# Performance work log

Measured on AMD Instinct MI355X. Metric: run time of the kernel, lower is better.

The kernel has to match this reference:

```python
import jax, jax.numpy as jnp
import numpy as np
from jax import lax

_MS_SSIM_WEIGHTS = [0.0448, 0.2856, 0.3001, 0.2363, 0.1333]
LEVELS = 5
WINDOW_SIZE = 11
SIGMA = 1.5
DATA_RANGE = 2.0


def _gaussian_kernel(size, sigma, channels):
    x = jnp.arange(size, dtype=jnp.float32) - size // 2
    g = jnp.exp(-x ** 2 / (2.0 * sigma ** 2))
    g = g / g.sum()
    k2d = jnp.outer(g, g)  # [size, size]
    # depthwise kernel: [C, 1, size, size] (OIHW with feature_group_count=C)
    return jnp.broadcast_to(k2d[None, None], (channels, 1, size, size))


def _depthwise_conv(x, kernel, pad):
    C = x.shape[1]
    return lax.conv_general_dilated(
        x, kernel,
        window_strides=(1, 1),
        padding=[(pad, pad), (pad, pad)],
        dimension_numbers=('NCHW', 'OIHW', 'NCHW'),
        feature_group_count=C)


def _avg_pool2(x):
    s = lax.reduce_window(x, 0.0, lax.add, (1, 1, 2, 2), (1, 1, 2, 2), 'VALID')
    return s * 0.25


def _ssim(x, y, window_size=WINDOW_SIZE, sigma=SIGMA, data_range=DATA_RANGE):
    K1, K2 = 0.01, 0.03
    C1 = (K1 * data_range) ** 2
    C2 = (K2 * data_range) ** 2
    kernel = _gaussian_kernel(window_size, sigma, x.shape[1])
    pad = window_size // 2
    mu1 = _depthwise_conv(x, kernel, pad)
    mu2 = _depthwise_conv(y, kernel, pad)
    mu1_sq = mu1 * mu1
    mu2_sq = mu2 * mu2
    mu1_mu2 = mu1 * mu2
    sig1_sq = _depthwise_conv(x * x, kernel, pad) - mu1_sq
    sig2_sq = _depthwise_conv(y * y, kernel, pad) - mu2_sq
    sig12 = _depthwise_conv(x * y, kernel, pad) - mu1_mu2
    num = (2.0 * mu1_mu2 + C1) * (2.0 * sig12 + C2)
    den = (mu1_sq + mu2_sq + C1) * (sig1_sq + sig2_sq + C2)
    ssim_map = num / (den + 1e-8)
    return ssim_map.mean()


def setup_inputs() -> dict:
    key = jax.random.key(0)
    k1, k2 = jax.random.split(key)
    pred = jax.random.normal(k1, (16, 3, 512, 512), dtype=jnp.float32)
    target = jax.random.normal(k2, (16, 3, 512, 512), dtype=jnp.float32)
    return {"pred": pred, "target": target}


def reference(pred, target):
    weights = jnp.asarray(_MS_SSIM_WEIGHTS[:LEVELS], dtype=jnp.float32)
    weights = weights / weights.sum()
    ms_ssim_val = jnp.zeros((), dtype=jnp.float32)
    x, y = pred, target
    for i in range(LEVELS):
        s = _ssim(x, y)
        ms_ssim_val = ms_ssim_val + weights[i] * s
        if i < LEVELS - 1:
            x = _avg_pool2(x)
            y = _avg_pool2(y)
    return 1.0 - ms_ssim_val
```

## Files before the change

### kernel.cpp

```cpp
#include <hip/hip_runtime.h>


#define TW 64
#define NIMG 48
#define P2 63
#define P1 62
#define NSLOT 256
#define SSTRIDE 16

typedef float v2f __attribute__((ext_vector_type(2)));

template <int TH>
__global__ __launch_bounds__(256, 2) void ssim_level_kernel(
    const float* __restrict__ x, const float* __restrict__ y,
    long imgStride, int rowStride,
    float* __restrict__ dsx, float* __restrict__ dsy,
    long dsImgStride, int dsRowStride,
    const float* __restrict__ zpad,
    float* __restrict__ slots, int H, int W, int pad, int do_ds)
{
    constexpr int HHALO = TH + 10;
    constexpr int RPT   = TH / 4;

    const float G[11] = {
        0.00102839f, 0.00759877f, 0.03600077f, 0.10936069f, 0.21300539f,
        0.26601173f, 0.21300539f, 0.10936069f, 0.03600077f, 0.00759877f,
        0.00102839f};
    const float C1 = 4.0e-4f;
    const float C2 = 3.6e-3f;

    __shared__ __align__(16) v2f   sm01[HHALO * P2];
    __shared__ __align__(16) v2f   sm23[HHALO * P2];
    __shared__ __align__(16) float sm4 [HHALO * P1];

    const int t   = threadIdx.x;
    const int img = blockIdx.z;
    const int C0  = blockIdx.x * TW;
    const int R0  = blockIdx.y * TH;
    const float* xi = x + (long)img * imgStride;
    const float* yi = y + (long)img * imgStride;

    if (do_ds) {
        const int dsW = W >> 1, dsH = H >> 1;
        const long dbase = (long)img * dsImgStride;
        for (int i = t; i < (TH / 2) * 32; i += 256) {
            const int dr = i >> 5, dc = i & 31;
            const int gr2 = (R0 >> 1) + dr;
            const int gc2 = (C0 >> 1) + dc;
            if (gr2 < dsH && gc2 < dsW) {
                const float* sx = xi + (long)(2 * gr2) * rowStride + 2 * gc2;
                const float* sy = yi + (long)(2 * gr2) * rowStride + 2 * gc2;
                const float2 a0 = *reinterpret_cast<const float2*>(sx);
                const float2 a1 = *reinterpret_cast<const float2*>(sx + rowStride);
                const float2 b0 = *reinterpret_cast<const float2*>(sy);
                const float2 b1 = *reinterpret_cast<const float2*>(sy + rowStride);
                const long o = dbase + (long)gr2 * dsRowStride + gc2;
                dsx[o] = 0.25f * (a0.x + a0.y + a1.x + a1.y);
                dsy[o] = 0.25f * (b0.x + b0.y + b1.x + b1.y);
            }
            if (gr2 < dsH && dc < 8) {
                if (blockIdx.x == 0) {
                    const long o = dbase + (long)gr2 * dsRowStride + (dc - 8);
                    dsx[o] = 0.0f; dsy[o] = 0.0f;
                }
                if (blockIdx.x == gridDim.x - 1) {
                    const long o = dbase + (long)gr2 * dsRowStride + (dsW + dc);
                    dsx[o] = 0.0f; dsy[o] = 0.0f;
                }
            }
        }
    }

    const bool fastp = pad || ((C0 >= 8) && (C0 + TW + 8 <= W));
    for (int s = t; s < HHALO * 8; s += 256) {
        const int r  = s % HHALO;
        const int q  = s / HHALO;
        const int gr = R0 + r - 5;
        const bool rok = ((unsigned)gr < (unsigned)H);
        const int gc0 = C0 + (q << 3) - 8;

        float xv[24], yv[24];
        if (fastp) {
            const float* px = rok ? (xi + (long)gr * rowStride + gc0) : zpad;
            const float* py = rok ? (yi + (long)gr * rowStride + gc0) : zpad;
#pragma unroll
            for (int v = 0; v < 6; ++v) {
                const float4 a = reinterpret_cast<const float4*>(px)[v];
                const float4 b = reinterpret_cast<const float4*>(py)[v];
                xv[4 * v + 0] = a.x; xv[4 * v + 1] = a.y;
                xv[4 * v + 2] = a.z; xv[4 * v + 3] = a.w;
                yv[4 * v + 0] = b.x; yv[4 * v + 1] = b.y;
                yv[4 * v + 2] = b.z; yv[4 * v + 3] = b.w;
            }
        } else {
            const float* xrow = xi + (long)gr * rowStride;
            const float* yrow = yi + (long)gr * rowStride;
#pragma unroll
            for (int k = 3; k < 21; ++k) {
                const int gc = gc0 + k;
                const bool ok = rok && ((unsigned)gc < (unsigned)W);
                xv[k] = ok ? xrow[gc] : 0.0f;
                yv[k] = ok ? yrow[gc] : 0.0f;
            }
        }

        v2f w2[18]; float xy[18];
#pragma unroll
        for (int k = 0; k < 18; ++k) {
            const float a = xv[k + 3], b = yv[k + 3];
            v2f w; w.x = a * a; w.y = b * b;
            w2[k] = w; xy[k] = a * b;
        }

        const int cb = (q << 3);
#pragma unroll
        for (int j = 0; j < 8; ++j) {
            v2f s01 = {0.f, 0.f}, s23 = {0.f, 0.f};
            float s4 = 0.f;
#pragma unroll
            for (int k = 0; k < 11; ++k) {
                const float g = G[k];
                v2f w; w.x = xv[j + k + 3]; w.y = yv[j + k + 3];
                s01 += w * g;
                s23 += w2[j + k] * g;
                s4   = fmaf(g, xy[j + k], s4);
            }
            sm01[r * P2 + cb + j] = s01;
            sm23[r * P2 + cb + j] = s23;
            sm4 [r * P1 + cb + j] = s4;
        }
    }
    __syncthreads();

    const int c   = t & 63;
    const int rr0 = (t >> 6) * RPT;
    v2f acc01[RPT], acc23[RPT];
    float acc4[RPT];
    {
        v2f hv[RPT + 10];
#pragma unroll
        for (int k = 0; k < RPT + 10; ++k) hv[k] = sm01[(rr0 + k) * P2 + c];
#pragma unroll
        for (int i = 0; i < RPT; ++i) {
            v2f a = {0.f, 0.f};
#pragma unroll
            for (int k = 0; k < 11; ++k) a += hv[i + k] * G[k];
            acc01[i] = a;
        }
#pragma unroll
        for (int k = 0; k < RPT + 10; ++k) hv[k] = sm23[(rr0 + k) * P2 + c];
#pragma unroll
        for (int i = 0; i < RPT; ++i) {
            v2f a = {0.f, 0.f};
#pragma unroll
            for (int k = 0; k < 11; ++k) a += hv[i + k] * G[k];
            acc23[i] = a;
        }
    }
    {
        float hs[RPT + 10];
#pragma unroll
        for (int k = 0; k < RPT + 10; ++k) hs[k] = sm4[(rr0 + k) * P1 + c];
#pragma unroll
        for (int i = 0; i < RPT; ++i) {
            float a = 0.f;
#pragma unroll
            for (int k = 0; k < 11; ++k) a = fmaf(G[k], hs[i + k], a);
            acc4[i] = a;
        }
    }

    float local = 0.f;
    const int gc = C0 + c;
#pragma unroll
    for (int i = 0; i < RPT; ++i) {
        const int gr2 = R0 + rr0 + i;
        if (gr2 < H && gc < W) {
            const float mu1 = acc01[i].x, mu2 = acc01[i].y;
            const float mu1s = mu1 * mu1, mu2s = mu2 * mu2, m12 = mu1 * mu2;
            const float s1  = acc23[i].x - mu1s;
            const float s2  = acc23[i].y - mu2s;
            const float s12 = acc4[i] - m12;
            const float num = (2.f * m12 + C1) * (2.f * s12 + C2);
            const float den = (mu1s + mu2s + C1) * (s1 + s2 + C2);
            local += num * __builtin_amdgcn_rcpf(den + 1e-8f);
        }
    }

#pragma unroll
    for (int off = 32; off > 0; off >>= 1) local += __shfl_down(local, off, 64);
    if ((t & 63) == 0) {
        const int bid = (blockIdx.z * gridDim.y + blockIdx.y) * gridDim.x + blockIdx.x;
        const int slot = ((bid << 2) | (t >> 6)) & (NSLOT - 1);
        atomicAdd(slots + slot * SSTRIDE, local);
    }
}

__global__ void finalize_kernel(const float* __restrict__ slots,
                                float* __restrict__ out)
{
    const int t = threadIdx.x;
    const float w[5] = {0.0448f, 0.2856f, 0.3001f, 0.2363f, 0.1333f};
    const float wsum = w[0] + w[1] + w[2] + w[3] + w[4];
    float acc = 0.f;
#pragma unroll
    for (int lvl = 0; lvl < 5; ++lvl) {
        const int d = 512 >> lvl;
        const float cnt = (float)NIMG * (float)d * (float)d;
        acc += (w[lvl] / wsum) / cnt * slots[(lvl * NSLOT + t) * SSTRIDE];
    }
#pragma unroll
    for (int off = 32; off > 0; off >>= 1) acc += __shfl_down(acc, off, 64);
    __shared__ float p[4];
    if ((t & 63) == 0) p[t >> 6] = acc;
    __syncthreads();
    if (t == 0) out[0] = 1.0f - (p[0] + p[1] + p[2] + p[3]);
}

extern "C" void kernel_launch(void* const* d_in, const int* in_sizes, int n_in,
                              void* d_out, int out_size, void* d_ws, size_t ws_size,
                              hipStream_t stream)
{
    const float* pred = (const float*)d_in[0];
    const float* targ = (const float*)d_in[1];
    float* out = (float*)d_out;
    float* ws  = (float*)d_ws;

    const long S1 = 256L * 272, S2 = 128L * 144, S3 = 64L * 80, S4 = 32L * 48;

    float* slots = ws;
    float* zpad  = slots + 5 * NSLOT * SSTRIDE;
    float* x1 = zpad + 640;
    float* y1 = x1 + NIMG * S1;
    float* x2 = y1 + NIMG * S1;
    float* y2 = x2 + NIMG * S2;
    float* x3 = y2 + NIMG * S2;
    float* y3 = x3 + NIMG * S3;
    float* x4 = y3 + NIMG * S3;
    float* y4 = x4 + NIMG * S4;

    hipMemsetAsync(ws, 0, (size_t)(5 * NSLOT * SSTRIDE + 640) * sizeof(float), stream);

    { dim3 g(8, 16, NIMG);
      ssim_level_kernel<32><<<g, 256, 0, stream>>>(pred, targ, 512L * 512, 512,
          x1 + 8, y1 + 8, S1, 272, zpad, slots + 0 * NSLOT * SSTRIDE, 512, 512, 0, 1); }
    { dim3 g(4, 8, NIMG);
      ssim_level_kernel<32><<<g, 256, 0, stream>>>(x1 + 8, y1 + 8, S1, 272,
          x2 + 8, y2 + 8, S2, 144, zpad, slots + 1 * NSLOT * SSTRIDE, 256, 256, 1, 1); }
    { dim3 g(2, 16, NIMG);
      ssim_level_kernel<8><<<g, 256, 0, stream>>>(x2 + 8, y2 + 8, S2, 144,
          x3 + 8, y3 + 8, S3, 80, zpad, slots + 2 * NSLOT * SSTRIDE, 128, 128, 1, 1); }
    { dim3 g(1, 8, NIMG);
      ssim_level_kernel<8><<<g, 256, 0, stream>>>(x3 + 8, y3 + 8, S3, 80,
          x4 + 8, y4 + 8, S4, 48, zpad, slots + 3 * NSLOT * SSTRIDE, 64, 64, 1, 1); }
    { dim3 g(1, 4, NIMG);
      ssim_level_kernel<8><<<g, 256, 0, stream>>>(x4 + 8, y4 + 8, S4, 48,
          nullptr, nullptr, 0, 0, zpad, slots + 4 * NSLOT * SSTRIDE, 32, 32, 1, 0); }

    finalize_kernel<<<1, 256, 0, stream>>>(slots, out);
}
```

Measured before the change: 283.6 us.

## Fuse pyramid pooling into level-0 kernel and merge remaining levels into one launch

The level-0 SSIM kernel now streams 128-row strips with a 42-row ring buffer in shared memory and fuses the four-level 2x2 average-pool pyramid into a single pass using shuffles. Levels 1-4 are merged into one launch with a flattened tile index. The three horizontal-conv planes are packed into a single float4 (x, y, x²+y², xy) with XOR swizzling, and the block size drops to 128 threads. The intent is to cut launch count, repeated downsample reads and halo recomputation, at the cost of more barriers per strip and lower per-block parallelism.

```diff
diff --git a/kernel.cpp b/kernel.cpp
--- a/kernel.cpp
+++ b/kernel.cpp
@@ -1,198 +1,342 @@
 #include <hip/hip_runtime.h>
 
 
-#define TW 64
+#define TW 32
+#define NTHR 128
 #define NIMG 48
-#define P2 63
-#define P1 62
+#define WIN 42
+#define PQ  32
 #define NSLOT 256
 #define SSTRIDE 16
 
-typedef float v2f __attribute__((ext_vector_type(2)));
-
-template <int TH>
-__global__ __launch_bounds__(256, 2) void ssim_level_kernel(
+#define RS1 272
+#define RS2 144
+#define RS3 80
+#define RS4 48
+#define IS0 (512L*512)
+#define IS1 (256L*272)
+#define IS2 (128L*144)
+#define IS3 (64L*80)
+#define IS4 (32L*48)
+
+typedef float v4f __attribute__((ext_vector_type(4)));
+
+struct Pyr {
+    float *x1, *y1, *x2, *y2, *x3, *y3, *x4, *y4;
+};
+
+__device__ __forceinline__ void h_load(
+    const float* __restrict__ xi, const float* __restrict__ yi,
+    const float* __restrict__ zpad, int gr, int gc0, int H, int W,
+    bool fastp, int rowStride, float* xv, float* yv)
+{
+    const bool rok = ((unsigned)gr < (unsigned)H);
+    if (fastp) {
+        const float* px = rok ? (xi + (long)gr * rowStride + gc0) : zpad;
+        const float* py = rok ? (yi + (long)gr * rowStride + gc0) : zpad;
+#pragma unroll
+        for (int v = 0; v < 6; ++v) {
+            const float4 a = reinterpret_cast<const float4*>(px)[v];
+            const float4 b = reinterpret_cast<const float4*>(py)[v];
+            xv[4*v+0]=a.x; xv[4*v+1]=a.y; xv[4*v+2]=a.z; xv[4*v+3]=a.w;
+            yv[4*v+0]=b.x; yv[4*v+1]=b.y; yv[4*v+2]=b.z; yv[4*v+3]=b.w;
+        }
+    } else {
+        const float* xrow = xi + (long)gr * rowStride;
+        const float* yrow = yi + (long)gr * rowStride;
+#pragma unroll
+        for (int k = 3; k < 21; ++k) {
+            const int gc = gc0 + k;
+            const bool ok = rok && ((unsigned)gc < (unsigned)W);
+            xv[k] = ok ? xrow[gc] : 0.0f;
+            yv[k] = ok ? yrow[gc] : 0.0f;
+        }
+    }
+}
+
+__device__ __forceinline__ void h_conv_write(
+    const float* xv, const float* yv, v4f* smA, int slot, int cb,
+    const float* G)
+{
+    v4f s[8];
+#pragma unroll
+    for (int j = 0; j < 8; ++j) s[j] = {0.f, 0.f, 0.f, 0.f};
+#pragma unroll
+    for (int m = 0; m < 18; ++m) {
+        const float a = xv[m+3], b = yv[m+3];
+        v4f w; w.x = a; w.y = b; w.z = a*a + b*b; w.w = a*b;
+#pragma unroll
+        for (int j = 0; j < 8; ++j) {
+            if (j <= m && m - j <= 10) {
+                s[j] += w * G[m - j];
+            }
+        }
+    }
+    const int u = slot & 31;
+#pragma unroll
+    for (int j = 0; j < 8; ++j)
+        smA[slot * PQ + ((cb + j) ^ u)] = s[j];
+}
+
+__device__ __forceinline__ float v_phase(
+    const v4f* smA, int vb, int c, int rr0, int R0, int C0, int H, int W,
+    const float* G)
+{
+    const float C1 = 4.0e-4f;
+    const float C2 = 3.6e-3f;
+    v4f acc[8];
+#pragma unroll
+    for (int i = 0; i < 8; ++i) acc[i] = {0.f, 0.f, 0.f, 0.f};
+    int sl = vb;
+#pragma unroll
+    for (int k = 0; k < 18; ++k) {
+        const v4f h = smA[sl * PQ + (c ^ (sl & 31))];
+#pragma unroll
+        for (int i = 0; i < 8; ++i) {
+            if (i <= k && k - i <= 10) {
+                acc[i] += h * G[k - i];
+            }
+        }
+        sl = (sl + 1 == WIN) ? 0 : sl + 1;
+    }
+    float local = 0.f;
+    const int gc = C0 + c;
+#pragma unroll
+    for (int i = 0; i < 8; ++i) {
+        const int gr2 = R0 + rr0 + i;
+        if (gr2 < H && gc < W) {
+            const float mu1 = acc[i].x, mu2 = acc[i].y;
+            const float mu1s = mu1*mu1, mu2s = mu2*mu2, m12 = mu1*mu2;
+            const float ssum = acc[i].z - mu1s - mu2s;
+            const float s12  = acc[i].w - m12;
+            const float num = (2.f * m12 + C1) * (2.f * s12 + C2);
+            const float den = (mu1s + mu2s + C1) * (ssum + C2);
+            local += num * __builtin_amdgcn_rcpf(den + 1e-8f);
+        }
+    }
+    return local;
+}
+
+__device__ __forceinline__ void pool_tree(
+    const float* __restrict__ xi, const float* __restrict__ yi,
+    int t, int R0, int C0, int z, const Pyr& p, int bx)
+{
+    const int r = t >> 3, c2 = t & 7;
+    const int gr = R0 + 4 * r;
+    const int gc = C0 + 4 * c2;
+
+    float4 ax[4], ay[4];
+#pragma unroll
+    for (int rr = 0; rr < 4; ++rr) {
+        ax[rr] = *reinterpret_cast<const float4*>(xi + (long)(gr+rr)*512 + gc);
+        ay[rr] = *reinterpret_cast<const float4*>(yi + (long)(gr+rr)*512 + gc);
+    }
+    float qx[2][2], qy[2][2];
+#pragma unroll
+    for (int i = 0; i < 2; ++i) {
+        qx[i][0] = 0.25f*(ax[2*i].x+ax[2*i].y+ax[2*i+1].x+ax[2*i+1].y);
+        qx[i][1] = 0.25f*(ax[2*i].z+ax[2*i].w+ax[2*i+1].z+ax[2*i+1].w);
+        qy[i][0] = 0.25f*(ay[2*i].x+ay[2*i].y+ay[2*i+1].x+ay[2*i+1].y);
+        qy[i][1] = 0.25f*(ay[2*i].z+ay[2*i].w+ay[2*i+1].z+ay[2*i+1].w);
+    }
+    float* x1p = p.x1 + z*IS1;  float* y1p = p.y1 + z*IS1;
+    float* x2p = p.x2 + z*IS2;  float* y2p = p.y2 + z*IS2;
+    float* x3p = p.x3 + z*IS3;  float* y3p = p.y3 + z*IS3;
+    float* x4p = p.x4 + z*IS4;  float* y4p = p.y4 + z*IS4;
+
+    const int r1 = (R0 >> 1) + 2*r, c1 = (C0 >> 1) + 2*c2;
+#pragma unroll
+    for (int i = 0; i < 2; ++i) {
+        *reinterpret_cast<float2*>(x1p + (long)(r1+i)*RS1 + c1) =
+            make_float2(qx[i][0], qx[i][1]);
+        *reinterpret_cast<float2*>(y1p + (long)(r1+i)*RS1 + c1) =
+            make_float2(qy[i][0], qy[i][1]);
+    }
+    const float v2x = 0.25f*(qx[0][0]+qx[0][1]+qx[1][0]+qx[1][1]);
+    const float v2y = 0.25f*(qy[0][0]+qy[0][1]+qy[1][0]+qy[1][1]);
+    x2p[(long)((R0>>2)+r)*RS2 + (C0>>2)+c2] = v2x;
+    y2p[(long)((R0>>2)+r)*RS2 + (C0>>2)+c2] = v2y;
+    const float v3x = 0.25f*(v2x + __shfl_down(v2x,1,64)
+                           + __shfl_down(v2x,8,64) + __shfl_down(v2x,9,64));
+    const float v3y = 0.25f*(v2y + __shfl_down(v2y,1,64)
+                           + __shfl_down(v2y,8,64) + __shfl_down(v2y,9,64));
+    if (!(r & 1) && !(c2 & 1)) {
+        x3p[(long)((R0>>3)+(r>>1))*RS3 + (C0>>3)+(c2>>1)] = v3x;
+        y3p[(long)((R0>>3)+(r>>1))*RS3 + (C0>>3)+(c2>>1)] = v3y;
+    }
+    const float v4x = 0.25f*(v3x + __shfl_down(v3x,2,64)
+                           + __shfl_down(v3x,16,64) + __shfl_down(v3x,18,64));
+    const float v4y = 0.25f*(v3y + __shfl_down(v3y,2,64)
+                           + __shfl_down(v3y,16,64) + __shfl_down(v3y,18,64));
+    if (!(r & 3) && !(c2 & 3)) {
+        x4p[(long)((R0>>4)+(r>>2))*RS4 + (C0>>4)+(c2>>2)] = v4x;
+        y4p[(long)((R0>>4)+(r>>2))*RS4 + (C0>>4)+(c2>>2)] = v4y;
+    }
+    if (bx == 0) {
+#pragma unroll
+        for (int i = 0; i < 2; ++i) {
+            x1p[(long)(r1+i)*RS1 + (c2-8)] = 0.f;
+            y1p[(long)(r1+i)*RS1 + (c2-8)] = 0.f;
+        }
+        x2p[(long)((R0>>2)+r)*RS2 + (c2-8)] = 0.f;
+        y2p[(long)((R0>>2)+r)*RS2 + (c2-8)] = 0.f;
+        if (r < 4) { x3p[(long)((R0>>3)+r)*RS3 + (c2-8)] = 0.f;
+                     y3p[(long)((R0>>3)+r)*RS3 + (c2-8)] = 0.f; }
+        if (r < 2) { x4p[(long)((R0>>4)+r)*RS4 + (c2-8)] = 0.f;
+                     y4p[(long)((R0>>4)+r)*RS4 + (c2-8)] = 0.f; }
+    }
+    if (bx == 15) {
+#pragma unroll
+        for (int i = 0; i < 2; ++i) {
+            x1p[(long)(r1+i)*RS1 + 256 + c2] = 0.f;
+            y1p[(long)(r1+i)*RS1 + 256 + c2] = 0.f;
+        }
+        x2p[(long)((R0>>2)+r)*RS2 + 128 + c2] = 0.f;
+        y2p[(long)((R0>>2)+r)*RS2 + 128 + c2] = 0.f;
+        if (r < 4) { x3p[(long)((R0>>3)+r)*RS3 + 64 + c2] = 0.f;
+                     y3p[(long)((R0>>3)+r)*RS3 + 64 + c2] = 0.f; }
+        if (r < 2) { x4p[(long)((R0>>4)+r)*RS4 + 32 + c2] = 0.f;
+                     y4p[(long)((R0>>4)+r)*RS4 + 32 + c2] = 0.f; }
+    }
+}
+
+__global__ __launch_bounds__(NTHR, 2) void ssim_l0_kernel(
     const float* __restrict__ x, const float* __restrict__ y,
-    long imgStride, int rowStride,
-    float* __restrict__ dsx, float* __restrict__ dsy,
-    long dsImgStride, int dsRowStride,
-    const float* __restrict__ zpad,
-    float* __restrict__ slots, int H, int W, int pad, int do_ds)
-{
-    constexpr int HHALO = TH + 10;
-    constexpr int RPT   = TH / 4;
-
+    Pyr p, const float* __restrict__ zpad, float* __restrict__ slots)
+{
     const float G[11] = {
         0.00102839f, 0.00759877f, 0.03600077f, 0.10936069f, 0.21300539f,
         0.26601173f, 0.21300539f, 0.10936069f, 0.03600077f, 0.00759877f,
         0.00102839f};
-    const float C1 = 4.0e-4f;
-    const float C2 = 3.6e-3f;
-
-    __shared__ __align__(16) v2f   sm01[HHALO * P2];
-    __shared__ __align__(16) v2f   sm23[HHALO * P2];
-    __shared__ __align__(16) float sm4 [HHALO * P1];
-
-    const int t   = threadIdx.x;
-    const int img = blockIdx.z;
-    const int C0  = blockIdx.x * TW;
-    const int R0  = blockIdx.y * TH;
-    const float* xi = x + (long)img * imgStride;
-    const float* yi = y + (long)img * imgStride;
-
-    if (do_ds) {
-        const int dsW = W >> 1, dsH = H >> 1;
-        const long dbase = (long)img * dsImgStride;
-        for (int i = t; i < (TH / 2) * 32; i += 256) {
-            const int dr = i >> 5, dc = i & 31;
-            const int gr2 = (R0 >> 1) + dr;
-            const int gc2 = (C0 >> 1) + dc;
-            if (gr2 < dsH && gc2 < dsW) {
-                const float* sx = xi + (long)(2 * gr2) * rowStride + 2 * gc2;
-                const float* sy = yi + (long)(2 * gr2) * rowStride + 2 * gc2;
-                const float2 a0 = *reinterpret_cast<const float2*>(sx);
-                const float2 a1 = *reinterpret_cast<const float2*>(sx + rowStride);
-                const float2 b0 = *reinterpret_cast<const float2*>(sy);
-                const float2 b1 = *reinterpret_cast<const float2*>(sy + rowStride);
-                const long o = dbase + (long)gr2 * dsRowStride + gc2;
-                dsx[o] = 0.25f * (a0.x + a0.y + a1.x + a1.y);
-                dsy[o] = 0.25f * (b0.x + b0.y + b1.x + b1.y);
-            }
-            if (gr2 < dsH && dc < 8) {
-                if (blockIdx.x == 0) {
-                    const long o = dbase + (long)gr2 * dsRowStride + (dc - 8);
-                    dsx[o] = 0.0f; dsy[o] = 0.0f;
-                }
-                if (blockIdx.x == gridDim.x - 1) {
-                    const long o = dbase + (long)gr2 * dsRowStride + (dsW + dc);
-                    dsx[o] = 0.0f; dsy[o] = 0.0f;
-                }
-            }
-        }
-    }
-
-    const bool fastp = pad || ((C0 >= 8) && (C0 + TW + 8 <= W));
-    for (int s = t; s < HHALO * 8; s += 256) {
-        const int r  = s % HHALO;
-        const int q  = s / HHALO;
-        const int gr = R0 + r - 5;
-        const bool rok = ((unsigned)gr < (unsigned)H);
-        const int gc0 = C0 + (q << 3) - 8;
-
+
+    __shared__ __align__(16) v4f smA[WIN * PQ];
+
+    const int t    = threadIdx.x;
+    const int bid  = blockIdx.x;
+    const int tile = (bid & 7) * 384 + (bid >> 3);
+    const int bx   = tile & 15;
+    const int by   = (tile >> 4) & 3;
+    const int z    = tile >> 6;
+    const int C0   = bx * TW;
+    const int S0   = by * 128;
+    const float* xi = x + (long)z * IS0;
+    const float* yi = y + (long)z * IS0;
+    const bool fastp = (C0 >= 8) && (C0 + TW + 8 <= 512);
+
+    for (int s = t; s < WIN * 4; s += NTHR) {
+        const int r = s % WIN, q = s / WIN;
+        float pxv[24], pyv[24];
+        h_load(xi, yi, zpad, S0 + r - 5, C0 + (q << 3) - 8, 512, 512, fastp,
+               512, pxv, pyv);
+        h_conv_write(pxv, pyv, smA, r, q << 3, G);
+    }
+    __syncthreads();
+
+    const int c    = t & 31;
+    const int rr0  = (t >> 5) * 8;
+    const int hr   = t & 31, hq = t >> 5;
+    const int hgc0 = C0 + (hq << 3) - 8;
+    int wslot = hr, vb = rr0;
+    float local = 0.f;
+
+    for (int tt = 0; tt < 3; ++tt) {
+        const int R0 = S0 + 32 * tt;
         float xv[24], yv[24];
-        if (fastp) {
-            const float* px = rok ? (xi + (long)gr * rowStride + gc0) : zpad;
-            const float* py = rok ? (yi + (long)gr * rowStride + gc0) : zpad;
-#pragma unroll
-            for (int v = 0; v < 6; ++v) {
-                const float4 a = reinterpret_cast<const float4*>(px)[v];
-                const float4 b = reinterpret_cast<const float4*>(py)[v];
-                xv[4 * v + 0] = a.x; xv[4 * v + 1] = a.y;
-                xv[4 * v + 2] = a.z; xv[4 * v + 3] = a.w;
-                yv[4 * v + 0] = b.x; yv[4 * v + 1] = b.y;
-                yv[4 * v + 2] = b.z; yv[4 * v + 3] = b.w;
-            }
-        } else {
-            const float* xrow = xi + (long)gr * rowStride;
-            const float* yrow = yi + (long)gr * rowStride;
-#pragma unroll
-            for (int k = 3; k < 21; ++k) {
-                const int gc = gc0 + k;
-                const bool ok = rok && ((unsigned)gc < (unsigned)W);
-                xv[k] = ok ? xrow[gc] : 0.0f;
-                yv[k] = ok ? yrow[gc] : 0.0f;
-            }
-        }
-
-        v2f w2[18]; float xy[18];
-#pragma unroll
-        for (int k = 0; k < 18; ++k) {
-            const float a = xv[k + 3], b = yv[k + 3];
-            v2f w; w.x = a * a; w.y = b * b;
-            w2[k] = w; xy[k] = a * b;
-        }
-
-        const int cb = (q << 3);
-#pragma unroll
-        for (int j = 0; j < 8; ++j) {
-            v2f s01 = {0.f, 0.f}, s23 = {0.f, 0.f};
-            float s4 = 0.f;
-#pragma unroll
-            for (int k = 0; k < 11; ++k) {
-                const float g = G[k];
-                v2f w; w.x = xv[j + k + 3]; w.y = yv[j + k + 3];
-                s01 += w * g;
-                s23 += w2[j + k] * g;
-                s4   = fmaf(g, xy[j + k], s4);
-            }
-            sm01[r * P2 + cb + j] = s01;
-            sm23[r * P2 + cb + j] = s23;
-            sm4 [r * P1 + cb + j] = s4;
-        }
-    }
-    __syncthreads();
-
-    const int c   = t & 63;
-    const int rr0 = (t >> 6) * RPT;
-    v2f acc01[RPT], acc23[RPT];
-    float acc4[RPT];
+        h_load(xi, yi, zpad, R0 + 37 + hr, hgc0, 512, 512, fastp, 512, xv, yv);
+        local += v_phase(smA, vb, c, rr0, R0, C0, 512, 512, G);
+        if (t < 64) pool_tree(xi, yi, t, R0, C0, z, p, bx);
+        __syncthreads();
+        h_conv_write(xv, yv, smA, wslot, hq << 3, G);
+        __syncthreads();
+        wslot += 32; if (wslot >= WIN) wslot -= WIN;
+        vb    += 32; if (vb    >= WIN) vb    -= WIN;
+    }
     {
-        v2f hv[RPT + 10];
-#pragma unroll
-        for (int k = 0; k < RPT + 10; ++k) hv[k] = sm01[(rr0 + k) * P2 + c];
-#pragma unroll
-        for (int i = 0; i < RPT; ++i) {
-            v2f a = {0.f, 0.f};
-#pragma unroll
-            for (int k = 0; k < 11; ++k) a += hv[i + k] * G[k];
-            acc01[i] = a;
-        }
-#pragma unroll
-        for (int k = 0; k < RPT + 10; ++k) hv[k] = sm23[(rr0 + k) * P2 + c];
-#pragma unroll
-        for (int i = 0; i < RPT; ++i) {
-            v2f a = {0.f, 0.f};
-#pragma unroll
-            for (int k = 0; k < 11; ++k) a += hv[i + k] * G[k];
-            acc23[i] = a;
-        }
-    }
-    {
-        float hs[RPT + 10];
-#pragma unroll
-        for (int k = 0; k < RPT + 10; ++k) hs[k] = sm4[(rr0 + k) * P1 + c];
-#pragma unroll
-        for (int i = 0; i < RPT; ++i) {
-            float a = 0.f;
-#pragma unroll
-            for (int k = 0; k < 11; ++k) a = fmaf(G[k], hs[i + k], a);
-            acc4[i] = a;
-        }
-    }
-
-    float local = 0.f;
-    const int gc = C0 + c;
-#pragma unroll
-    for (int i = 0; i < RPT; ++i) {
-        const int gr2 = R0 + rr0 + i;
-        if (gr2 < H && gc < W) {
-            const float mu1 = acc01[i].x, mu2 = acc01[i].y;
-            const float mu1s = mu1 * mu1, mu2s = mu2 * mu2, m12 = mu1 * mu2;
-            const float s1  = acc23[i].x - mu1s;
-            const float s2  = acc23[i].y - mu2s;
-            const float s12 = acc4[i] - m12;
-            const float num = (2.f * m12 + C1) * (2.f * s12 + C2);
-            const float den = (mu1s + mu2s + C1) * (s1 + s2 + C2);
-            local += num * __builtin_amdgcn_rcpf(den + 1e-8f);
-        }
+        const int R0 = S0 + 96;
+        local += v_phase(smA, vb, c, rr0, R0, C0, 512, 512, G);
+        if (t < 64) pool_tree(xi, yi, t, R0, C0, z, p, bx);
     }
 
 #pragma unroll
     for (int off = 32; off > 0; off >>= 1) local += __shfl_down(local, off, 64);
     if ((t & 63) == 0) {
-        const int bid = (blockIdx.z * gridDim.y + blockIdx.y) * gridDim.x + blockIdx.x;
-        const int slot = ((bid << 2) | (t >> 6)) & (NSLOT - 1);
+        const int slot = ((tile << 1) | (t >> 6)) & (NSLOT - 1);
         atomicAdd(slots + slot * SSTRIDE, local);
+    }
+}
+
+__global__ __launch_bounds__(NTHR, 2) void ssim_lvls_kernel(
+    Pyr p, const float* __restrict__ zpad, float* __restrict__ slots)
+{
+    const float G[11] = {
+        0.00102839f, 0.00759877f, 0.03600077f, 0.10936069f, 0.21300539f,
+        0.26601173f, 0.21300539f, 0.10936069f, 0.03600077f, 0.00759877f,
+        0.00102839f};
+
+    __shared__ __align__(16) v4f smA[WIN * PQ];
+
+    const int t    = threadIdx.x;
+    const int bid  = blockIdx.x;
+    const int tile = (bid % 8) * 318 + (bid / 8);
+
+    const float* xi; const float* yi;
+    int rowStride, H, C0, S0, nsub, lvl, rem;
+    if (tile < 1536) {
+        rem = tile; lvl = 1; nsub = 2;
+        const int bx = rem & 7, by = (rem >> 3) & 3, z = rem >> 5;
+        xi = p.x1 + (long)z * IS1; yi = p.y1 + (long)z * IS1;
+        rowStride = RS1; H = 256; C0 = bx * TW; S0 = by * 64;
+    } else if (tile < 2304) {
+        rem = tile - 1536; lvl = 2; nsub = 1;
+        const int bx = rem & 3, by = (rem >> 2) & 3, z = rem >> 4;
+        xi = p.x2 + (long)z * IS2; yi = p.y2 + (long)z * IS2;
+        rowStride = RS2; H = 128; C0 = bx * TW; S0 = by * 32;
+    } else if (tile < 2496) {
+        rem = tile - 2304; lvl = 3; nsub = 1;
+        const int bx = rem & 1, by = (rem >> 1) & 1, z = rem >> 2;
+        xi = p.x3 + (long)z * IS3; yi = p.y3 + (long)z * IS3;
+        rowStride = RS3; H = 64; C0 = bx * TW; S0 = by * 32;
+    } else {
+        rem = tile - 2496; lvl = 4; nsub = 1;
+        const int z = rem;
+        xi = p.x4 + (long)z * IS4; yi = p.y4 + (long)z * IS4;
+        rowStride = RS4; H = 32; C0 = 0; S0 = 0;
+    }
+
+    for (int s = t; s < WIN * 4; s += NTHR) {
+        const int r = s % WIN, q = s / WIN;
+        float pxv[24], pyv[24];
+        h_load(xi, yi, zpad, S0 + r - 5, C0 + (q << 3) - 8, H, H, true,
+               rowStride, pxv, pyv);
+        h_conv_write(pxv, pyv, smA, r, q << 3, G);
+    }
+    __syncthreads();
+
+    const int c    = t & 31;
+    const int rr0  = (t >> 5) * 8;
+    const int hr   = t & 31, hq = t >> 5;
+    int wslot = hr, vb = rr0;
+    float local = 0.f;
+
+    for (int tt = 0; tt < nsub - 1; ++tt) {
+        const int R0 = S0 + 32 * tt;
+        float xv[24], yv[24];
+        h_load(xi, yi, zpad, R0 + 37 + hr, C0 + (hq << 3) - 8, H, H, true,
+               rowStride, xv, yv);
+        local += v_phase(smA, vb, c, rr0, R0, C0, H, H, G);
+        __syncthreads();
+        h_conv_write(xv, yv, smA, wslot, hq << 3, G);
+        __syncthreads();
+        wslot += 32; if (wslot >= WIN) wslot -= WIN;
+        vb    += 32; if (vb    >= WIN) vb    -= WIN;
+    }
+    local += v_phase(smA, vb, c, rr0, S0 + 32 * (nsub - 1), C0, H, H, G);
+
+#pragma unroll
+    for (int off = 32; off > 0; off >>= 1) local += __shfl_down(local, off, 64);
+    if ((t & 63) == 0) {
+        const int slot = ((rem << 1) | (t >> 6)) & (NSLOT - 1);
+        atomicAdd(slots + ((long)lvl * NSLOT + slot) * SSTRIDE, local);
     }
 }
 
@@ -211,10 +355,10 @@
     }
 #pragma unroll
     for (int off = 32; off > 0; off >>= 1) acc += __shfl_down(acc, off, 64);
-    __shared__ float p[4];
-    if ((t & 63) == 0) p[t >> 6] = acc;
+    __shared__ float pp[4];
+    if ((t & 63) == 0) pp[t >> 6] = acc;
     __syncthreads();
-    if (t == 0) out[0] = 1.0f - (p[0] + p[1] + p[2] + p[3]);
+    if (t == 0) out[0] = 1.0f - (pp[0] + pp[1] + pp[2] + pp[3]);
 }
 
 extern "C" void kernel_launch(void* const* d_in, const int* in_sizes, int n_in,
@@ -226,36 +370,31 @@
     float* out = (float*)d_out;
     float* ws  = (float*)d_ws;
 
-    const long S1 = 256L * 272, S2 = 128L * 144, S3 = 64L * 80, S4 = 32L * 48;
-
     float* slots = ws;
     float* zpad  = slots + 5 * NSLOT * SSTRIDE;
-    float* x1 = zpad + 640;
-    float* y1 = x1 + NIMG * S1;
-    float* x2 = y1 + NIMG * S1;
-    float* y2 = x2 + NIMG * S2;
-    float* x3 = y2 + NIMG * S2;
-    float* y3 = x3 + NIMG * S3;
-    float* x4 = y3 + NIMG * S3;
-    float* y4 = x4 + NIMG * S4;
-
-    hipMemsetAsync(ws, 0, (size_t)(5 * NSLOT * SSTRIDE + 640) * sizeof(float), stream);
-
-    { dim3 g(8, 16, NIMG);
-      ssim_level_kernel<32><<<g, 256, 0, stream>>>(pred, targ, 512L * 512, 512,
-          x1 + 8, y1 + 8, S1, 272, zpad, slots + 0 * NSLOT * SSTRIDE, 512, 512, 0, 1); }
-    { dim3 g(4, 8, NIMG);
-      ssim_level_kernel<32><<<g, 256, 0, stream>>>(x1 + 8, y1 + 8, S1, 272,
-          x2 + 8, y2 + 8, S2, 144, zpad, slots + 1 * NSLOT * SSTRIDE, 256, 256, 1, 1); }
-    { dim3 g(2, 16, NIMG);
-      ssim_level_kernel<8><<<g, 256, 0, stream>>>(x2 + 8, y2 + 8, S2, 144,
-          x3 + 8, y3 + 8, S3, 80, zpad, slots + 2 * NSLOT * SSTRIDE, 128, 128, 1, 1); }
-    { dim3 g(1, 8, NIMG);
-      ssim_level_kernel<8><<<g, 256, 0, stream>>>(x3 + 8, y3 + 8, S3, 80,
-          x4 + 8, y4 + 8, S4, 48, zpad, slots + 3 * NSLOT * SSTRIDE, 64, 64, 1, 1); }
-    { dim3 g(1, 4, NIMG);
-      ssim_level_kernel<8><<<g, 256, 0, stream>>>(x4 + 8, y4 + 8, S4, 48,
-          nullptr, nullptr, 0, 0, zpad, slots + 4 * NSLOT * SSTRIDE, 32, 32, 1, 0); }
+
+    Pyr p;
+    p.x1 = zpad + 640 + 8;
+    p.y1 = p.x1 + NIMG * IS1;
+    p.x2 = p.y1 + NIMG * IS1 - 8 + 8;
+    p.x2 = p.y1 + NIMG * IS1;
+    {
+        float* b = zpad + 640;
+        p.x1 = b + 8;                 b += NIMG * IS1;
+        p.y1 = b + 8;                 b += NIMG * IS1;
+        p.x2 = b + 8;                 b += NIMG * IS2;
+        p.y2 = b + 8;                 b += NIMG * IS2;
+        p.x3 = b + 8;                 b += NIMG * IS3;
+        p.y3 = b + 8;                 b += NIMG * IS3;
+        p.x4 = b + 8;                 b += NIMG * IS4;
+        p.y4 = b + 8;
+    }
+
+    hipMemsetAsync(ws, 0, (size_t)(5 * NSLOT * SSTRIDE + 640) * sizeof(float),
+                   stream);
+
+    ssim_l0_kernel<<<dim3(3072), NTHR, 0, stream>>>(pred, targ, p, zpad, slots);
+    ssim_lvls_kernel<<<dim3(2544), NTHR, 0, stream>>>(p, zpad, slots);
 
     finalize_kernel<<<1, 256, 0, stream>>>(slots, out);
 }
```

Measured after the change: 233.5 us. 17.7% less time.
